# Optimization experiments

Hardware: AMD Instinct MI355X
Metric: run time of the kernel (lower is better)

Reference implementation:

```python
import jax, jax.numpy as jnp
import numpy as np
from jax import lax

# Fixed dims from MSSMamba defaults
B_, L_, DM = 2, 8192, 256
NH, HP, NS = 4, 64, 8          # nheads, headdim, d_state
DIN = NH * HP                  # d_inner = 256
DPROJ = 2 * DIN + 2 * NS + NH  # 532


def setup_inputs() -> dict:
    key = jax.random.key(0)
    ks = jax.random.split(key, 16)
    f = lambda k, s, sc=1.0: jax.random.normal(k, s, jnp.float32) * sc
    inp = {
        'x_H': f(ks[0], (B_, L_, DM)),
        'x_V': f(ks[1], (B_, L_, DM)),
        'W_in_H': f(ks[2], (DM, 2 * DPROJ), 0.05),
        'W_in_V': f(ks[3], (DM, 2 * DPROJ), 0.05),
        'W_out_HF': f(ks[4], (DIN, DM), 0.05),
        'W_out_HB': f(ks[5], (DIN, DM), 0.05),
        'W_out_VF': f(ks[6], (DIN, DM), 0.05),
        'W_out_VB': f(ks[7], (DIN, DM), 0.05),
        'W_out': f(ks[8], (4 * DM, DM), 0.05),
    }
    for i, nm in enumerate(['HF', 'HB', 'VF', 'VB']):
        kd = jax.random.fold_in(ks[9], i)
        ka = jax.random.fold_in(ks[10], i)
        inp['dt_bias_' + nm] = f(kd, (NH,), 0.1)
        inp['A_log_' + nm] = jnp.log(jax.random.uniform(ka, (NH,), jnp.float32, 1.0, 16.0))
        inp['D_' + nm] = jnp.ones((NH,), jnp.float32)
    # per-batch permutation mapping vertical position -> horizontal position
    inp['v2h'] = jax.vmap(lambda k: jax.random.permutation(k, L_))(
        jax.random.split(ks[11], B_)).astype(jnp.int32)
    return inp


def _scan_dir(zxbcdt, dt_bias, A_log, D):
    # zxbcdt: [b, l, DPROJ] -> Mamba2-style selective scan, ngroups=1
    z = zxbcdt[..., :DIN].reshape(B_, L_, NH, HP)
    xBC = jax.nn.silu(zxbcdt[..., DIN:DIN + DIN + 2 * NS])
    x = xBC[..., :DIN].reshape(B_, L_, NH, HP)
    Bm = xBC[..., DIN:DIN + NS]      # [b, l, n]
    Cm = xBC[..., DIN + NS:]         # [b, l, n]
    dt = jax.nn.softplus(zxbcdt[..., -NH:] + dt_bias)  # [b, l, h]
    A = -jnp.exp(A_log)              # [h]
    dA = jnp.exp(dt * A)             # [b, l, h]
    dBx = jnp.einsum('blh,bln,blhp->blhpn', dt, Bm, x)  # [b,l,h,p,n]

    def step(state, inp):
        dA_t, dBx_t, C_t = inp
        state = dA_t[..., None, None] * state + dBx_t   # [b,h,p,n]
        y_t = jnp.einsum('bhpn,bn->bhp', state, C_t)
        return state, y_t

    init = jnp.zeros((B_, NH, HP, NS), dt.dtype)
    _, ys = lax.scan(step, init, (jnp.moveaxis(dA, 1, 0),
                                  jnp.moveaxis(dBx, 1, 0),
                                  jnp.moveaxis(Cm, 1, 0)))
    y = jnp.moveaxis(ys, 0, 1) + D[None, None, :, None] * x  # skip D*x
    y = y * jax.nn.silu(z)                                   # gate
    return y.reshape(B_, L_, DIN)


def reference(x_H, x_V, W_in_H, W_in_V,
              dt_bias_HF, dt_bias_HB, dt_bias_VF, dt_bias_VB,
              A_log_HF, A_log_HB, A_log_VF, A_log_VB,
              D_HF, D_HB, D_VF, D_VB,
              W_out_HF, W_out_HB, W_out_VF, W_out_VB,
              W_out, v2h):
    zx_HF, zx_HB = jnp.split(x_H @ W_in_H, 2, axis=-1)
    zx_VF, zx_VB = jnp.split(x_V @ W_in_V, 2, axis=-1)
    # note: source applies out_proj_HB to the HF branch (kept faithful)
    y_HF = _scan_dir(zx_HF, dt_bias_HF, A_log_HF, D_HF) @ W_out_HB
    y_HB = _scan_dir(zx_HB[:, ::-1], dt_bias_HB, A_log_HB, D_HB)[:, ::-1] @ W_out_HF
    y_VF = _scan_dir(zx_VF, dt_bias_VF, A_log_VF, D_VF) @ W_out_VB
    y_VB = _scan_dir(zx_VB[:, ::-1], dt_bias_VB, A_log_VB, D_VB)[:, ::-1] @ W_out_VF
    # remap vertical-ordered outputs to horizontal ordering (scatter by v2h)
    bidx = jnp.arange(B_)[:, None]
    y_VF = jnp.zeros_like(y_VF).at[bidx, v2h].set(y_VF)
    y_VB = jnp.zeros_like(y_VB).at[bidx, v2h].set(y_VB)
    cat = jnp.concatenate([y_HF, y_HB, y_VF, y_VB], axis=-1)  # [b, l, 4*d_model]
    return jax.nn.silu(cat) @ W_out
```

## Files before the change

kernel.cpp:

```cpp
#include <hip/hip_runtime.h>
#include <hip/hip_bf16.h>

#define B_N 2
#define L_N 8192
#define ROWS 16384
#define CHUNK 32
#define NCHUNK 256
#define NPAD 1152

typedef __bf16 bf16x8 __attribute__((ext_vector_type(8)));
typedef float f32x4 __attribute__((ext_vector_type(4)));

__device__ __forceinline__ float siluf(float v) {
  return v * __builtin_amdgcn_rcpf(1.f + __expf(-v));
}
__device__ __forceinline__ float softplusf_(float v) {
  return fmaxf(v, 0.f) + log1pf(__expf(-fabsf(v)));
}
__device__ __forceinline__ unsigned short f2bf(float v) {
  union { __bf16 b; unsigned short u; } x;
  x.b = (__bf16)v;
  return x.u;
}
__device__ __forceinline__ float bf2f(unsigned short u) {
  union { unsigned u; float f; } x; x.u = ((unsigned)u) << 16;
  return x.f;
}

__device__ __forceinline__ void gload_lds16(const unsigned short* g, unsigned short* l) {
  __builtin_amdgcn_global_load_lds(
      (const __attribute__((address_space(1))) unsigned int*)g,
      (__attribute__((address_space(3))) unsigned int*)l, 16, 0, 0);
}

struct P4 { const float* p[4]; };
struct ScanConsts {
  const float* dt_bias[4];
  const float* A_log[4];
  const float* D[4];
};

__global__ __launch_bounds__(256) void k_prep(
    const float* __restrict__ xH, const float* __restrict__ xV,
    const float* __restrict__ WH, const float* __restrict__ WV,
    P4 ws, const float* __restrict__ W_out, const int* __restrict__ v2h, ScanConsts sc,
    unsigned short* __restrict__ xbf, float* __restrict__ dtv_arr, float* __restrict__ dA_arr,
    unsigned short* __restrict__ Wt_in, unsigned short* __restrict__ Wt_dirs,
    unsigned short* __restrict__ Wt_fin, int* __restrict__ inv) {
  __shared__ float xs[32][257];
  __shared__ float Wsm[8][260];
  int bid = blockIdx.x;
  int tid = threadIdx.x;
  if (bid < 1024) {
    const int mat = bid >> 9;
    const float* x = mat ? xV : xH;
    const float* W = mat ? WV : WH;
    const int r0 = (bid & 511) * 32;
    for (int i = tid; i < 2048; i += 256) {
      int c = i >> 8, k = i & 255;
      int sl = c >> 2, h = c & 3;
      Wsm[c][k] = W[(long)k * 1064 + sl * 532 + 528 + h];
    }
    for (int i = tid; i < 32 * 64; i += 256) {
      int rl = i >> 6, kq = (i & 63) * 4;
      float4 v = *(const float4*)(x + (long)(r0 + rl) * 256 + kq);
      xs[rl][kq + 0] = v.x; xs[rl][kq + 1] = v.y; xs[rl][kq + 2] = v.z; xs[rl][kq + 3] = v.w;
    }
    __syncthreads();
    for (int i = tid; i < 32 * 64; i += 256) {
      int rl = i >> 6, kq = (i & 63) * 4;
      ushort4 o;
      o.x = f2bf(xs[rl][kq + 0]);
      o.y = f2bf(xs[rl][kq + 1]);
      o.z = f2bf(xs[rl][kq + 2]);
      o.w = f2bf(xs[rl][kq + 3]);
      *(ushort4*)(xbf + (size_t)mat * ROWS * 256 + (long)(r0 + rl) * 256 + kq) = o;
    }
    const int rl = tid >> 3, c = tid & 7;
    float s = 0.f;
    #pragma unroll 8
    for (int k = 0; k < 256; ++k) s = fmaf(xs[rl][k], Wsm[c][k], s);
    const int sl = c >> 2, h = c & 3;
    const int dir = mat * 2 + sl;
    float dtv = softplusf_(s + sc.dt_bias[dir][h]);
    float dAv = __expf(dtv * (-__expf(sc.A_log[dir][h])));
    long o = ((long)dir * 4 + h) * ROWS + (r0 + rl);
    dtv_arr[o] = dtv;
    dA_arr[o] = dAv;
  } else if (bid < 3328) {
    int i = (bid - 1024) * 256 + tid;
    int z = i / (NPAD * 256);
    int rem = i - z * (NPAD * 256);
    int n = rem >> 8, k = rem & 255;
    const float* W = z ? WV : WH;
    int sl = n >= 544;
    int cc = n - (sl ? 544 : 0);
    float v = (cc < 532) ? W[(long)k * 1064 + sl * 532 + cc] : 0.f;
    Wt_in[i] = f2bf(v);
  } else if (bid < 4352) {
    int i = (bid - 3328) * 256 + tid;
    int d = i >> 16;
    int rem = i & 65535;
    int n = rem >> 8, k = rem & 255;
    Wt_dirs[i] = f2bf(ws.p[d][(long)k * 256 + n]);
  } else if (bid < 5376) {
    int i = (bid - 4352) * 256 + tid;
    int n = i >> 10, k = i & 1023;
    Wt_fin[i] = f2bf(W_out[(long)k * 256 + n]);
  } else {
    int m = (bid - 5376) * 256 + tid;
    if (m < ROWS) {
      int b = m >> 13;
      inv[b * L_N + v2h[m]] = m;
    }
  }
}

struct EpiIn {
  unsigned short* zraw;
  unsigned short* xraw;
  unsigned short* bc;
};

__global__ __launch_bounds__(256) void k_gemm_in(
    const unsigned short* __restrict__ Abase, const unsigned short* __restrict__ Btbase,
    EpiIn ep) {
  __shared__ unsigned short As[128 * 32];
  __shared__ unsigned short Bs[128 * 32];
  __shared__ unsigned short trs[4][16 * 72];
  const int tid = threadIdx.x;
  const int lane = tid & 63;
  const int wid = tid >> 6;
  const int wm = wid & 1, wn = wid >> 1;
  const int q = lane >> 4, r = lane & 15;
  const int m0 = blockIdx.x * 128;
  const int n0 = blockIdx.y * 128;
  const int z = blockIdx.z;
  const unsigned short* A = Abase + (long)z * ROWS * 256;
  const unsigned short* Bt = Btbase + (long)z * NPAD * 256;

  f32x4 acc[4][4] = {};
  const int swr = (r >> 1) & 3;

  for (int kt = 0; kt < 256; kt += 32) {
    #pragma unroll
    for (int i = 0; i < 2; ++i) {
      int idx = i * 256 + tid;
      int row = idx >> 2;
      int ch = (idx & 3) ^ ((row >> 1) & 3);
      gload_lds16(A + (long)(m0 + row) * 256 + kt + ch * 8,
                  &As[(size_t)(i * 256 + wid * 64) * 8]);
    }
    #pragma unroll
    for (int i = 0; i < 2; ++i) {
      int idx = i * 256 + tid;
      int row = idx >> 2;
      int ch = (idx & 3) ^ ((row >> 1) & 3);
      gload_lds16(Bt + (long)(n0 + row) * 256 + kt + ch * 8,
                  &Bs[(size_t)(i * 256 + wid * 64) * 8]);
    }
    __syncthreads();
    bf16x8 af[4], bfr[4];
    #pragma unroll
    for (int mi = 0; mi < 4; ++mi)
      af[mi] = *(const bf16x8*)&As[((wm * 64 + mi * 16 + r) * 4 + (q ^ swr)) * 8];
    #pragma unroll
    for (int ni = 0; ni < 4; ++ni)
      bfr[ni] = *(const bf16x8*)&Bs[((wn * 64 + ni * 16 + r) * 4 + (q ^ swr)) * 8];
    #pragma unroll
    for (int mi = 0; mi < 4; ++mi)
      #pragma unroll
      for (int ni = 0; ni < 4; ++ni)
        acc[mi][ni] = __builtin_amdgcn_mfma_f32_16x16x32_bf16(af[mi], bfr[ni], acc[mi][ni], 0, 0, 0);
    __syncthreads();
  }

  unsigned short* tr = trs[wid];
  #pragma unroll
  for (int mi = 0; mi < 4; ++mi) {
    #pragma unroll
    for (int ni = 0; ni < 4; ++ni)
      #pragma unroll
      for (int j = 0; j < 4; ++j)
        tr[(q * 4 + j) * 72 + ni * 16 + r] = f2bf(acc[mi][ni][j]);
    asm volatile("s_waitcnt lgkmcnt(0)" ::: "memory");
    #pragma unroll
    for (int pass = 0; pass < 2; ++pass) {
      int rl = pass * 8 + (lane >> 3);
      int c8 = (lane & 7) * 8;
      bf16x8 v = *(const bf16x8*)&tr[rl * 72 + c8];
      int row = m0 + wm * 64 + mi * 16 + rl;
      int col = n0 + wn * 64 + c8;
      int sl = col >= 544;
      int cc = col - (sl ? 544 : 0);
      if (cc < 528) {
        int dir = z * 2 + sl;
        if (cc < 256)
          *(bf16x8*)(ep.zraw + ((long)dir * ROWS + row) * 256 + cc) = v;
        else if (cc < 512)
          *(bf16x8*)(ep.xraw + ((long)dir * ROWS + row) * 256 + cc - 256) = v;
        else
          *(bf16x8*)(ep.bc + ((long)dir * ROWS + row) * 16 + cc - 512) = v;
      }
    }
    asm volatile("s_waitcnt lgkmcnt(0)" ::: "memory");
  }
}

__global__ __launch_bounds__(256) void k_fuse(
    const unsigned short* __restrict__ ybf,
    const unsigned short* __restrict__ Wt_dirs,
    const unsigned short* __restrict__ Wt_fin,
    const int* __restrict__ inv,
    unsigned short* __restrict__ pbuf) {
  __shared__ unsigned short smem[64 * 264 + 256 * 32];
  __shared__ int arow[64];
  unsigned short* Tl = smem;
  unsigned short* As1 = smem;
  unsigned short* Bs1 = smem + 64 * 264;
  const int tid = threadIdx.x;
  const int lane = tid & 63;
  const int wid = tid >> 6;
  const int q = lane >> 4, r = lane & 15;
  const int r0 = blockIdx.x * 64;
  const int pair = blockIdx.y;
  const int swr = (r >> 1) & 3;

  if (tid < 64) arow[tid] = pair ? inv[r0 + tid] : (r0 + tid);
  __syncthreads();

  f32x4 acc_o[4][4] = {};

  #pragma unroll
  for (int dd = 0; dd < 2; ++dd) {
    const int d = pair * 2 + dd;
    const unsigned short* yd = ybf + (long)d * ROWS * 256;
    const unsigned short* Wd = Wt_dirs + (long)d * 65536;

    f32x4 acc_t[4][4] = {};
    for (int kt = 0; kt < 256; kt += 32) {
      {
        int row = tid >> 2;
        int ch = (tid & 3) ^ ((row >> 1) & 3);
        gload_lds16(yd + (long)arow[row] * 256 + kt + ch * 8, &As1[(size_t)(wid * 64) * 8]);
      }
      #pragma unroll
      for (int i = 0; i < 4; ++i) {
        int idx = i * 256 + tid;
        int row = idx >> 2;
        int ch = (idx & 3) ^ ((row >> 1) & 3);
        gload_lds16(Wd + (long)row * 256 + kt + ch * 8,
                    &Bs1[(size_t)(i * 256 + wid * 64) * 8]);
      }
      __syncthreads();
      bf16x8 af[4], bfr[4];
      #pragma unroll
      for (int mi = 0; mi < 4; ++mi)
        af[mi] = *(const bf16x8*)&As1[((mi * 16 + r) * 4 + (q ^ swr)) * 8];
      #pragma unroll
      for (int ni = 0; ni < 4; ++ni)
        bfr[ni] = *(const bf16x8*)&Bs1[((wid * 64 + ni * 16 + r) * 4 + (q ^ swr)) * 8];
      #pragma unroll
      for (int mi = 0; mi < 4; ++mi)
        #pragma unroll
        for (int ni = 0; ni < 4; ++ni)
          acc_t[mi][ni] = __builtin_amdgcn_mfma_f32_16x16x32_bf16(af[mi], bfr[ni], acc_t[mi][ni], 0, 0, 0);
      __syncthreads();
    }
    #pragma unroll
    for (int mi = 0; mi < 4; ++mi)
      #pragma unroll
      for (int ni = 0; ni < 4; ++ni)
        #pragma unroll
        for (int j = 0; j < 4; ++j)
          Tl[(mi * 16 + q * 4 + j) * 264 + wid * 64 + ni * 16 + r] = f2bf(siluf(acc_t[mi][ni][j]));
    __syncthreads();
    for (int kt = 0; kt < 256; kt += 32) {
      #pragma unroll
      for (int i = 0; i < 4; ++i) {
        int idx = i * 256 + tid;
        int row = idx >> 2;
        int ch = (idx & 3) ^ ((row >> 1) & 3);
        gload_lds16(Wt_fin + (long)row * 1024 + d * 256 + kt + ch * 8,
                    &Bs1[(size_t)(i * 256 + wid * 64) * 8]);
      }
      __syncthreads();
      bf16x8 af[4], bfr[4];
      #pragma unroll
      for (int mi = 0; mi < 4; ++mi)
        af[mi] = *(const bf16x8*)&Tl[(mi * 16 + r) * 264 + kt + q * 8];
      #pragma unroll
      for (int ni = 0; ni < 4; ++ni)
        bfr[ni] = *(const bf16x8*)&Bs1[((wid * 64 + ni * 16 + r) * 4 + (q ^ swr)) * 8];
      #pragma unroll
      for (int mi = 0; mi < 4; ++mi)
        #pragma unroll
        for (int ni = 0; ni < 4; ++ni)
          acc_o[mi][ni] = __builtin_amdgcn_mfma_f32_16x16x32_bf16(af[mi], bfr[ni], acc_o[mi][ni], 0, 0, 0);
      __syncthreads();
    }
  }

  #pragma unroll
  for (int mi = 0; mi < 4; ++mi)
    #pragma unroll
    for (int ni = 0; ni < 4; ++ni)
      #pragma unroll
      for (int j = 0; j < 4; ++j)
        Tl[(mi * 16 + q * 4 + j) * 264 + wid * 64 + ni * 16 + r] = f2bf(acc_o[mi][ni][j]);
  asm volatile("s_waitcnt lgkmcnt(0)" ::: "memory");
  unsigned short* pout = pbuf + (long)pair * ROWS * 256;
  #pragma unroll
  for (int pass = 0; pass < 8; ++pass) {
    int rl = pass * 8 + (lane >> 3);
    int c8 = (lane & 7) * 8;
    bf16x8 v = *(const bf16x8*)&Tl[rl * 264 + wid * 64 + c8];
    *(bf16x8*)(pout + (long)(r0 + rl) * 256 + wid * 64 + c8) = v;
  }
}

__global__ void k_red(const unsigned short* __restrict__ pbuf, float* __restrict__ out) {
  int i = blockIdx.x * 256 + threadIdx.x;
  uint4 a = ((const uint4*)pbuf)[i];
  uint4 b = ((const uint4*)(pbuf + (size_t)ROWS * 256))[i];
  const unsigned short* au = (const unsigned short*)&a;
  const unsigned short* bu = (const unsigned short*)&b;
  float rr[8];
  #pragma unroll
  for (int j = 0; j < 8; ++j) rr[j] = bf2f(au[j]) + bf2f(bu[j]);
  ((float4*)out)[i * 2] = *(float4*)&rr[0];
  ((float4*)out)[i * 2 + 1] = *(float4*)&rr[4];
}

struct ScanP {
  const unsigned short* xraw;
  const unsigned short* zraw;
  const unsigned short* bc;
  const float* dtv;
  const float* dA;
  const float* D[4];
};

__global__ __launch_bounds__(64) void k_scan1(ScanP sp, float* __restrict__ S,
                                              float* __restrict__ P) {
  __shared__ __align__(16) float Bst[CHUNK][8];
  __shared__ float dAs[CHUNK];
  const int p = threadIdx.x;
  const int c = blockIdx.x;
  const int bh = blockIdx.y;
  const int d = blockIdx.z;
  const int b = bh >> 2, h = bh & 3;
  const int rev = d & 1;
  const int t0 = c * CHUNK;
  if (p < CHUNK) {
    const int t = t0 + p;
    const int l = rev ? (L_N - 1 - t) : t;
    const int row = (b << 13) + l;
    uint4 bv = *(const uint4*)(sp.bc + ((long)d * ROWS + row) * 16);
    const unsigned short* bu = (const unsigned short*)&bv;
    float dtvv = sp.dtv[((long)d * 4 + h) * ROWS + row];
    dAs[p] = sp.dA[((long)d * 4 + h) * ROWS + row];
    #pragma unroll
    for (int n = 0; n < 8; ++n) Bst[p][n] = siluf(bf2f(bu[n])) * dtvv;
  }
  __syncthreads();

  float st[8] = {0, 0, 0, 0, 0, 0, 0, 0};
  float cumdA = 1.f;
  const int l0 = rev ? (L_N - 1 - t0) : t0;
  const unsigned short* xp = sp.xraw + ((long)d * ROWS + (b << 13) + l0) * 256 + h * 64 + p;
  const long stp = rev ? -256L : 256L;

  unsigned short xa[8], xb[8];
  #pragma unroll
  for (int j = 0; j < 8; ++j) xa[j] = xp[(long)j * stp];
  #pragma unroll
  for (int g = 0; g < 4; ++g) {
    if (g < 3) {
      #pragma unroll
      for (int j = 0; j < 8; ++j) xb[j] = xp[(long)((g + 1) * 8 + j) * stp];
    }
    #pragma unroll
    for (int j = 0; j < 8; ++j) {
      int s = g * 8 + j;
      float x = siluf(bf2f(xa[j]));
      float dA = dAs[s];
      f32x4 B0 = *(const f32x4*)&Bst[s][0];
      f32x4 B1 = *(const f32x4*)&Bst[s][4];
      cumdA *= dA;
      st[0] = fmaf(dA, st[0], x * B0[0]);
      st[1] = fmaf(dA, st[1], x * B0[1]);
      st[2] = fmaf(dA, st[2], x * B0[2]);
      st[3] = fmaf(dA, st[3], x * B0[3]);
      st[4] = fmaf(dA, st[4], x * B1[0]);
      st[5] = fmaf(dA, st[5], x * B1[1]);
      st[6] = fmaf(dA, st[6], x * B1[2]);
      st[7] = fmaf(dA, st[7], x * B1[3]);
    }
    #pragma unroll
    for (int j = 0; j < 8; ++j) xa[j] = xb[j];
  }
  float* Sp = S + ((((long)d * NCHUNK + c) * 8 + bh) * 64 + p) * 8;
  #pragma unroll
  for (int n = 0; n < 8; ++n) Sp[n] = st[n];
  if (p == 0) P[((long)d * NCHUNK + c) * 8 + bh] = cumdA;
}

__global__ __launch_bounds__(512) void k_scan2(const float* __restrict__ S,
                                               const float* __restrict__ P,
                                               float* __restrict__ carry) {
  __shared__ float Pl[NCHUNK];
  const int tid = threadIdx.x;
  const int dbh = blockIdx.x;
  const int d = dbh >> 3, bh = dbh & 7;
  if (tid < NCHUNK) Pl[tid] = P[((long)d * NCHUNK + tid) * 8 + bh];
  __syncthreads();
  float cy = 0.f;
  carry[(((long)d * NCHUNK + 0) * 8 + bh) * 512 + tid] = 0.f;
  #pragma unroll 8
  for (int c = 1; c < NCHUNK; ++c) {
    const float Sv = S[(((long)d * NCHUNK + (c - 1)) * 8 + bh) * 512 + tid];
    cy = fmaf(Pl[c - 1], cy, Sv);
    carry[(((long)d * NCHUNK + c) * 8 + bh) * 512 + tid] = cy;
  }
}

__global__ __launch_bounds__(64) void k_scan3(ScanP sp, const float* __restrict__ carry,
                                              unsigned short* __restrict__ ybf) {
  __shared__ __align__(16) float Bst[CHUNK][8];
  __shared__ __align__(16) float Cst[CHUNK][8];
  __shared__ float dAs[CHUNK];
  const int p = threadIdx.x;
  const int c = blockIdx.x;
  const int bh = blockIdx.y;
  const int d = blockIdx.z;
  const int b = bh >> 2, h = bh & 3;
  const int rev = d & 1;
  const float Dv = sp.D[d][h];
  const int t0 = c * CHUNK;
  if (p < CHUNK) {
    const int t = t0 + p;
    const int l = rev ? (L_N - 1 - t) : t;
    const int row = (b << 13) + l;
    const unsigned short* bp = sp.bc + ((long)d * ROWS + row) * 16;
    uint4 bv = *(const uint4*)bp;
    uint4 cv = *(const uint4*)(bp + 8);
    const unsigned short* bu = (const unsigned short*)&bv;
    const unsigned short* cu = (const unsigned short*)&cv;
    float dtvv = sp.dtv[((long)d * 4 + h) * ROWS + row];
    dAs[p] = sp.dA[((long)d * 4 + h) * ROWS + row];
    #pragma unroll
    for (int n = 0; n < 8; ++n) Bst[p][n] = siluf(bf2f(bu[n])) * dtvv;
    #pragma unroll
    for (int n = 0; n < 8; ++n) Cst[p][n] = siluf(bf2f(cu[n]));
  }
  __syncthreads();

  float st[8];
  {
    const float* cp = carry + ((((long)d * NCHUNK + c) * 8 + bh) * 64 + p) * 8;
    #pragma unroll
    for (int n = 0; n < 8; ++n) st[n] = cp[n];
  }

  const int l0 = rev ? (L_N - 1 - t0) : t0;
  const long base = (long)(b << 13) + l0;
  const unsigned short* xp = sp.xraw + ((long)d * ROWS + base) * 256 + h * 64 + p;
  const unsigned short* zp = sp.zraw + ((long)d * ROWS + base) * 256 + h * 64 + p;
  unsigned short* yp = ybf + ((long)d * ROWS + base) * 256 + h * 64 + p;
  const long stp = rev ? -256L : 256L;

  unsigned short xa[8], xb[8], za[8], zb[8];
  #pragma unroll
  for (int j = 0; j < 8; ++j) { xa[j] = xp[(long)j * stp]; za[j] = zp[(long)j * stp]; }
  #pragma unroll
  for (int g = 0; g < 4; ++g) {
    if (g < 3) {
      #pragma unroll
      for (int j = 0; j < 8; ++j) {
        xb[j] = xp[(long)((g + 1) * 8 + j) * stp];
        zb[j] = zp[(long)((g + 1) * 8 + j) * stp];
      }
    }
    #pragma unroll
    for (int j = 0; j < 8; ++j) {
      int s = g * 8 + j;
      float x = siluf(bf2f(xa[j]));
      float zv = siluf(bf2f(za[j]));
      float dA = dAs[s];
      f32x4 B0 = *(const f32x4*)&Bst[s][0];
      f32x4 B1 = *(const f32x4*)&Bst[s][4];
      f32x4 C0 = *(const f32x4*)&Cst[s][0];
      f32x4 C1 = *(const f32x4*)&Cst[s][4];
      st[0] = fmaf(dA, st[0], x * B0[0]);
      st[1] = fmaf(dA, st[1], x * B0[1]);
      st[2] = fmaf(dA, st[2], x * B0[2]);
      st[3] = fmaf(dA, st[3], x * B0[3]);
      st[4] = fmaf(dA, st[4], x * B1[0]);
      st[5] = fmaf(dA, st[5], x * B1[1]);
      st[6] = fmaf(dA, st[6], x * B1[2]);
      st[7] = fmaf(dA, st[7], x * B1[3]);
      float y01 = fmaf(st[1], C0[1], st[0] * C0[0]);
      float y23 = fmaf(st[3], C0[3], st[2] * C0[2]);
      float y45 = fmaf(st[5], C1[1], st[4] * C1[0]);
      float y67 = fmaf(st[7], C1[3], st[6] * C1[2]);
      float y = (y01 + y23) + (y45 + y67);
      y = fmaf(Dv, x, y) * zv;
      yp[(long)s * stp] = f2bf(y);
    }
    #pragma unroll
    for (int j = 0; j < 8; ++j) { xa[j] = xb[j]; za[j] = zb[j]; }
  }
}

extern "C" void kernel_launch(void* const* d_in, const int* in_sizes, int n_in,
                              void* d_out, int out_size, void* d_ws, size_t ws_size,
                              hipStream_t stream) {
  const float* x_H = (const float*)d_in[0];
  const float* x_V = (const float*)d_in[1];
  const float* W_in_H = (const float*)d_in[2];
  const float* W_in_V = (const float*)d_in[3];
  const float* W_out_HF = (const float*)d_in[4];
  const float* W_out_HB = (const float*)d_in[5];
  const float* W_out_VF = (const float*)d_in[6];
  const float* W_out_VB = (const float*)d_in[7];
  const float* W_out = (const float*)d_in[8];
  const float* dt_bias_HF = (const float*)d_in[9];
  const float* A_log_HF = (const float*)d_in[10];
  const float* D_HF = (const float*)d_in[11];
  const float* dt_bias_HB = (const float*)d_in[12];
  const float* A_log_HB = (const float*)d_in[13];
  const float* D_HB = (const float*)d_in[14];
  const float* dt_bias_VF = (const float*)d_in[15];
  const float* A_log_VF = (const float*)d_in[16];
  const float* D_VF = (const float*)d_in[17];
  const float* dt_bias_VB = (const float*)d_in[18];
  const float* A_log_VB = (const float*)d_in[19];
  const float* D_VB = (const float*)d_in[20];
  const int* v2h = (const int*)d_in[21];

  char* ws = (char*)d_ws;
  size_t off = 0;
  auto alloc = [&](size_t bytes) {
    void* pp = ws + off;
    off = (off + bytes + 255) & ~(size_t)255;
    return pp;
  };
  unsigned short* xbf = (unsigned short*)alloc((size_t)2 * ROWS * 256 * 2);
  unsigned short* Wt_in = (unsigned short*)alloc((size_t)2 * NPAD * 256 * 2);
  unsigned short* Wt_dirs = (unsigned short*)alloc((size_t)4 * 65536 * 2);
  unsigned short* Wt_fin = (unsigned short*)alloc((size_t)256 * 1024 * 2);
  unsigned short* zraw = (unsigned short*)alloc((size_t)4 * ROWS * 256 * 2);
  unsigned short* xraw = (unsigned short*)alloc((size_t)4 * ROWS * 256 * 2);
  unsigned short* bc = (unsigned short*)alloc((size_t)4 * ROWS * 16 * 2);
  float* dtv_arr = (float*)alloc((size_t)16 * ROWS * 4);
  float* dA_arr = (float*)alloc((size_t)16 * ROWS * 4);
  unsigned short* ybf = (unsigned short*)alloc((size_t)4 * ROWS * 256 * 2);
  float* S = (float*)alloc((size_t)4 * NCHUNK * 8 * 512 * 4);
  float* P = (float*)alloc((size_t)4 * NCHUNK * 8 * 4);
  float* carry = (float*)alloc((size_t)4 * NCHUNK * 8 * 512 * 4);
  int* inv = (int*)alloc((size_t)ROWS * 4);
  unsigned short* pbuf = (unsigned short*)alloc((size_t)2 * ROWS * 256 * 2);

  ScanConsts sc;
  sc.dt_bias[0] = dt_bias_HF; sc.dt_bias[1] = dt_bias_HB;
  sc.dt_bias[2] = dt_bias_VF; sc.dt_bias[3] = dt_bias_VB;
  sc.A_log[0] = A_log_HF; sc.A_log[1] = A_log_HB;
  sc.A_log[2] = A_log_VF; sc.A_log[3] = A_log_VB;
  sc.D[0] = D_HF; sc.D[1] = D_HB; sc.D[2] = D_VF; sc.D[3] = D_VB;

  P4 wdirs;
  wdirs.p[0] = W_out_HB; wdirs.p[1] = W_out_HF; wdirs.p[2] = W_out_VB; wdirs.p[3] = W_out_VF;

  k_prep<<<5440, 256, 0, stream>>>(x_H, x_V, W_in_H, W_in_V, wdirs, W_out, v2h, sc,
                                   xbf, dtv_arr, dA_arr, Wt_in, Wt_dirs, Wt_fin, inv);

  EpiIn ep; ep.zraw = zraw; ep.xraw = xraw; ep.bc = bc;

  k_gemm_in<<<dim3(ROWS / 128, NPAD / 128, 2), 256, 0, stream>>>(xbf, Wt_in, ep);

  ScanP sp;
  sp.xraw = xraw; sp.zraw = zraw; sp.bc = bc; sp.dtv = dtv_arr; sp.dA = dA_arr;
  sp.D[0] = D_HF; sp.D[1] = D_HB; sp.D[2] = D_VF; sp.D[3] = D_VB;

  k_scan1<<<dim3(NCHUNK, 8, 4), 64, 0, stream>>>(sp, S, P);
  k_scan2<<<32, 512, 0, stream>>>(S, P, carry);
  k_scan3<<<dim3(NCHUNK, 8, 4), 64, 0, stream>>>(sp, carry, ybf);

  k_fuse<<<dim3(ROWS / 64, 2), 256, 0, stream>>>(ybf, Wt_dirs, Wt_fin, inv, pbuf);
  k_red<<<ROWS * 256 / 8 / 256, 256, 0, stream>>>(pbuf, (float*)d_out);

  (void)in_sizes; (void)n_in; (void)out_size; (void)ws_size;
}
```

Measured before the change: 265.2 us.

## Load k_fuse GEMM operands directly from global memory and use 8 waves

The k_fuse kernel stops staging the gathered activation rows and weight tiles through LDS with gload_lds and per-k-step barriers. Each wave now reads its MFMA fragments straight from global memory (and from L2 for the weights), and the block grows to 512 threads in a 2x4 wave grid with 32x64 tiles per wave. This removes LDS traffic and most barriers and aims for higher occupancy with launch_bounds(512,4). In exchange, global loads are uncoalesced fragment reads that depend on cache hits for the shared weights.

```diff
diff --git a/kernel.cpp b/kernel.cpp
--- a/kernel.cpp
+++ b/kernel.cpp
@@ -207,115 +207,98 @@
   }
 }
 
-__global__ __launch_bounds__(256) void k_fuse(
+__global__ __launch_bounds__(512, 4) void k_fuse(
     const unsigned short* __restrict__ ybf,
     const unsigned short* __restrict__ Wt_dirs,
     const unsigned short* __restrict__ Wt_fin,
     const int* __restrict__ inv,
     unsigned short* __restrict__ pbuf) {
-  __shared__ unsigned short smem[64 * 264 + 256 * 32];
+  __shared__ unsigned short Tl[64 * 264];
   __shared__ int arow[64];
-  unsigned short* Tl = smem;
-  unsigned short* As1 = smem;
-  unsigned short* Bs1 = smem + 64 * 264;
   const int tid = threadIdx.x;
   const int lane = tid & 63;
   const int wid = tid >> 6;
+  const int wm = wid & 1, wn = wid >> 1;
   const int q = lane >> 4, r = lane & 15;
   const int r0 = blockIdx.x * 64;
   const int pair = blockIdx.y;
-  const int swr = (r >> 1) & 3;
 
   if (tid < 64) arow[tid] = pair ? inv[r0 + tid] : (r0 + tid);
   __syncthreads();
 
-  f32x4 acc_o[4][4] = {};
+  long aoff[2];
+  #pragma unroll
+  for (int mi = 0; mi < 2; ++mi)
+    aoff[mi] = (long)arow[wm * 32 + mi * 16 + r] * 256 + q * 8;
+
+  f32x4 acc_o[2][4] = {};
 
   #pragma unroll
   for (int dd = 0; dd < 2; ++dd) {
     const int d = pair * 2 + dd;
     const unsigned short* yd = ybf + (long)d * ROWS * 256;
-    const unsigned short* Wd = Wt_dirs + (long)d * 65536;
-
-    f32x4 acc_t[4][4] = {};
+    const unsigned short* Wd = Wt_dirs + (long)d * 65536 + (long)(wn * 64) * 256 + q * 8;
+
+    f32x4 acc_t[2][4] = {};
+    #pragma unroll 2
     for (int kt = 0; kt < 256; kt += 32) {
-      {
-        int row = tid >> 2;
-        int ch = (tid & 3) ^ ((row >> 1) & 3);
-        gload_lds16(yd + (long)arow[row] * 256 + kt + ch * 8, &As1[(size_t)(wid * 64) * 8]);
-      }
-      #pragma unroll
-      for (int i = 0; i < 4; ++i) {
-        int idx = i * 256 + tid;
-        int row = idx >> 2;
-        int ch = (idx & 3) ^ ((row >> 1) & 3);
-        gload_lds16(Wd + (long)row * 256 + kt + ch * 8,
-                    &Bs1[(size_t)(i * 256 + wid * 64) * 8]);
-      }
-      __syncthreads();
-      bf16x8 af[4], bfr[4];
-      #pragma unroll
-      for (int mi = 0; mi < 4; ++mi)
-        af[mi] = *(const bf16x8*)&As1[((mi * 16 + r) * 4 + (q ^ swr)) * 8];
+      bf16x8 af[2], bfr[4];
+      #pragma unroll
+      for (int mi = 0; mi < 2; ++mi)
+        af[mi] = *(const bf16x8*)(yd + aoff[mi] + kt);
       #pragma unroll
       for (int ni = 0; ni < 4; ++ni)
-        bfr[ni] = *(const bf16x8*)&Bs1[((wid * 64 + ni * 16 + r) * 4 + (q ^ swr)) * 8];
-      #pragma unroll
-      for (int mi = 0; mi < 4; ++mi)
+        bfr[ni] = *(const bf16x8*)(Wd + (long)(ni * 16 + r) * 256 + kt);
+      #pragma unroll
+      for (int mi = 0; mi < 2; ++mi)
         #pragma unroll
         for (int ni = 0; ni < 4; ++ni)
           acc_t[mi][ni] = __builtin_amdgcn_mfma_f32_16x16x32_bf16(af[mi], bfr[ni], acc_t[mi][ni], 0, 0, 0);
-      __syncthreads();
-    }
-    #pragma unroll
-    for (int mi = 0; mi < 4; ++mi)
+    }
+    __syncthreads();
+    #pragma unroll
+    for (int mi = 0; mi < 2; ++mi)
       #pragma unroll
       for (int ni = 0; ni < 4; ++ni)
         #pragma unroll
         for (int j = 0; j < 4; ++j)
-          Tl[(mi * 16 + q * 4 + j) * 264 + wid * 64 + ni * 16 + r] = f2bf(siluf(acc_t[mi][ni][j]));
+          Tl[(wm * 32 + mi * 16 + q * 4 + j) * 264 + wn * 64 + ni * 16 + r] =
+              f2bf(siluf(acc_t[mi][ni][j]));
     __syncthreads();
+    const unsigned short* Wf = Wt_fin + (long)(wn * 64) * 1024 + d * 256 + q * 8;
+    #pragma unroll 2
     for (int kt = 0; kt < 256; kt += 32) {
-      #pragma unroll
-      for (int i = 0; i < 4; ++i) {
-        int idx = i * 256 + tid;
-        int row = idx >> 2;
-        int ch = (idx & 3) ^ ((row >> 1) & 3);
-        gload_lds16(Wt_fin + (long)row * 1024 + d * 256 + kt + ch * 8,
-                    &Bs1[(size_t)(i * 256 + wid * 64) * 8]);
-      }
-      __syncthreads();
-      bf16x8 af[4], bfr[4];
-      #pragma unroll
-      for (int mi = 0; mi < 4; ++mi)
-        af[mi] = *(const bf16x8*)&Tl[(mi * 16 + r) * 264 + kt + q * 8];
+      bf16x8 af[2], bfr[4];
+      #pragma unroll
+      for (int mi = 0; mi < 2; ++mi)
+        af[mi] = *(const bf16x8*)&Tl[(wm * 32 + mi * 16 + r) * 264 + kt + q * 8];
       #pragma unroll
       for (int ni = 0; ni < 4; ++ni)
-        bfr[ni] = *(const bf16x8*)&Bs1[((wid * 64 + ni * 16 + r) * 4 + (q ^ swr)) * 8];
-      #pragma unroll
-      for (int mi = 0; mi < 4; ++mi)
+        bfr[ni] = *(const bf16x8*)(Wf + (long)(ni * 16 + r) * 1024 + kt);
+      #pragma unroll
+      for (int mi = 0; mi < 2; ++mi)
         #pragma unroll
         for (int ni = 0; ni < 4; ++ni)
           acc_o[mi][ni] = __builtin_amdgcn_mfma_f32_16x16x32_bf16(af[mi], bfr[ni], acc_o[mi][ni], 0, 0, 0);
-      __syncthreads();
-    }
-  }
-
-  #pragma unroll
-  for (int mi = 0; mi < 4; ++mi)
+    }
+  }
+
+  __syncthreads();
+  #pragma unroll
+  for (int mi = 0; mi < 2; ++mi)
     #pragma unroll
     for (int ni = 0; ni < 4; ++ni)
       #pragma unroll
       for (int j = 0; j < 4; ++j)
-        Tl[(mi * 16 + q * 4 + j) * 264 + wid * 64 + ni * 16 + r] = f2bf(acc_o[mi][ni][j]);
+        Tl[(wm * 32 + mi * 16 + q * 4 + j) * 264 + wn * 64 + ni * 16 + r] = f2bf(acc_o[mi][ni][j]);
   asm volatile("s_waitcnt lgkmcnt(0)" ::: "memory");
   unsigned short* pout = pbuf + (long)pair * ROWS * 256;
   #pragma unroll
-  for (int pass = 0; pass < 8; ++pass) {
+  for (int pass = 0; pass < 4; ++pass) {
     int rl = pass * 8 + (lane >> 3);
     int c8 = (lane & 7) * 8;
-    bf16x8 v = *(const bf16x8*)&Tl[rl * 264 + wid * 64 + c8];
-    *(bf16x8*)(pout + (long)(r0 + rl) * 256 + wid * 64 + c8) = v;
+    bf16x8 v = *(const bf16x8*)&Tl[(wm * 32 + rl) * 264 + wn * 64 + c8];
+    *(bf16x8*)(pout + (long)(r0 + wm * 32 + rl) * 256 + wn * 64 + c8) = v;
   }
 }
 
@@ -587,7 +570,7 @@
   k_scan2<<<32, 512, 0, stream>>>(S, P, carry);
   k_scan3<<<dim3(NCHUNK, 8, 4), 64, 0, stream>>>(sp, carry, ybf);
 
-  k_fuse<<<dim3(ROWS / 64, 2), 256, 0, stream>>>(ybf, Wt_dirs, Wt_fin, inv, pbuf);
+  k_fuse<<<dim3(ROWS / 64, 2), 512, 0, stream>>>(ybf, Wt_dirs, Wt_fin, inv, pbuf);
   k_red<<<ROWS * 256 / 8 / 256, 256, 0, stream>>>(pbuf, (float*)d_out);
 
   (void)in_sizes; (void)n_in; (void)out_size; (void)ws_size;
```

After: 314.5 us. +18.6%, slower.
